# Kernel tuning notes

Measured on AMD Instinct MI355X. Metric: run time of the kernel, lower is better.

The kernel has to match this reference:

```python
import jax, jax.numpy as jnp
import numpy as np

B, T, N, PREV_DIM, CURR_DIM = 8, 32, 500, 200, 128
HEADS, UNITS, MSG_UNITS = 4, 64, 64


def setup_inputs() -> dict:
    key = jax.random.key(0)
    k = jax.random.split(key, 6)
    prev_features = jax.random.normal(k[0], (B, N, PREV_DIM), jnp.float32)
    curr_hidden = jax.random.normal(k[1], (B, T, N, CURR_DIM), jnp.float32)
    # glorot-ish small params
    W_src = jax.random.normal(k[2], (HEADS, PREV_DIM, UNITS), jnp.float32) * 0.05
    W_dst = jax.random.normal(k[3], (HEADS, PREV_DIM, UNITS), jnp.float32) * 0.05
    a = jax.random.normal(k[4], (HEADS, UNITS, 1), jnp.float32) * 0.1
    W_msg = jax.random.normal(k[5], (HEADS, CURR_DIM, MSG_UNITS), jnp.float32) * 0.05
    return {"prev_features": prev_features, "curr_hidden": curr_hidden,
            "W_src": W_src, "W_dst": W_dst, "a": a, "W_msg": W_msg}


def reference(prev_features, curr_hidden, W_src, W_dst, a, W_msg):
    # prev_features: [B, N, Dp]; curr_hidden: [B, T, N, Dc]
    heads = W_src.shape[0]
    head_outputs = []
    for h in range(heads):  # small fixed loop over heads (as in original)
        h_src = jnp.einsum('bnd,du->bnu', prev_features, W_src[h])  # [B,N,U]
        h_dst = jnp.einsum('bnd,du->bnu', prev_features, W_dst[h])  # [B,N,U]
        # GATv2 additive scoring: lrelu(src_i + dst_j) . a   -> [B,N,N]
        pairwise = jax.nn.leaky_relu(h_src[:, :, None, :] + h_dst[:, None, :, :], 0.2)
        scores = jnp.einsum('bnmu,u->bnm', pairwise, a[h, :, 0])
        attn = jax.nn.softmax(scores, axis=-1)  # [B,N,N]; dropout is identity at inference
        msg = jnp.einsum('btnd,du->btnu', curr_hidden, W_msg[h])  # [B,T,N,Mu]
        # same graph applied at every timestep (tf.repeat + batched matmul)
        h_prime = jnp.einsum('bnm,btmu->btnu', attn, msg)  # [B,T,N,Mu]
        head_outputs.append(h_prime)
    return jnp.mean(jnp.stack(head_outputs, axis=-1), axis=-1)
```

## Files before the change

kernel.cpp:

```cpp
#include <hip/hip_runtime.h>

#define B_ 8
#define T_ 32
#define N_ 500
#define DP 200
#define DC 128
#define H_ 4
#define U_ 64
#define NP 512
#define COLS (T_ * U_)
#define K4 (H_ * NP)

typedef __attribute__((ext_vector_type(8))) short bf16x8;
typedef __attribute__((ext_vector_type(4))) float f32x4;

__device__ __forceinline__ ushort f2bf(float f) {
    unsigned u = __float_as_uint(f);
    unsigned r = (u + 0x7FFFu + ((u >> 16) & 1u)) >> 16;
    return (ushort)r;
}

__global__ void zero_fill(uint4* __restrict__ p, int n16) {
    int i = blockIdx.x * blockDim.x + threadIdx.x;
    int stride = gridDim.x * blockDim.x;
    uint4 z; z.x = 0; z.y = 0; z.z = 0; z.w = 0;
    for (; i < n16; i += stride) p[i] = z;
}

__global__ void prep_wT(const float* __restrict__ Wmsg, ushort* __restrict__ WT) {
    int idx = blockIdx.x * 256 + threadIdx.x;
    int h = idx >> 13, u = (idx >> 7) & 63, d = idx & 127;
    WT[idx] = f2bf(0.25f * Wmsg[((size_t)h * DC + d) * U_ + u]);
}

__global__ void __launch_bounds__(512) proj_all(
    const float* __restrict__ prev, const float* __restrict__ Wsrc,
    const float* __restrict__ Wdst, float* __restrict__ hsrc,
    float* __restrict__ hdst)
{
    __shared__ float rows[4 * DP];
    const int tid = threadIdx.x;
    const int bn0 = blockIdx.x * 4;
    for (int e = tid; e < 4 * DP; e += 512) rows[e] = prev[(size_t)bn0 * DP + e];
    __syncthreads();
    const int u = tid & 63;
    const int h = (tid >> 6) & 3;
    const int isdst = tid >> 8;
    const float* W = (isdst ? Wdst : Wsrc) + (size_t)h * DP * U_;
    float a0 = 0.f, a1 = 0.f, a2 = 0.f, a3 = 0.f;
#pragma unroll 4
    for (int d = 0; d < DP; ++d) {
        float w = W[d * U_ + u];
        a0 = fmaf(rows[d], w, a0);
        a1 = fmaf(rows[DP + d], w, a1);
        a2 = fmaf(rows[2 * DP + d], w, a2);
        a3 = fmaf(rows[3 * DP + d], w, a3);
    }
    float acc[4] = {a0, a1, a2, a3};
    float* o = isdst ? hdst : hsrc;
#pragma unroll
    for (int r = 0; r < 4; ++r) {
        int bn = bn0 + r, b = bn / N_, n = bn - b * N_;
        o[(((size_t)b * H_ + h) * N_ + n) * U_ + u] = acc[r];
    }
}

__global__ void __launch_bounds__(512) attn_softmax4(
    const float* __restrict__ hsrc, const float* __restrict__ hdst,
    const float* __restrict__ a_all, ushort* __restrict__ attnB)
{
    const int i0 = blockIdx.x * 4, b = blockIdx.y, h = blockIdx.z;
    const int tid = threadIdx.x;
    __shared__ float s_src[4][U_];
    __shared__ float s_a[U_];
    __shared__ float red[32];
    __shared__ float s_mx[4], s_rs[4];

    if (tid < 256)
        s_src[tid >> 6][tid & 63] =
            hsrc[(((size_t)b * H_ + h) * N_ + i0 + (tid >> 6)) * U_ + (tid & 63)];
    else if (tid < 320)
        s_a[tid - 256] = a_all[h * U_ + (tid - 256)];
    __syncthreads();

    const int j = tid;
    const bool valid = j < N_;
    const float4* dp =
        (const float4*)&hdst[(((size_t)b * H_ + h) * N_ + (valid ? j : 0)) * U_];

    float av0 = 0.f, av1 = 0.f, av2 = 0.f, av3 = 0.f;
    float q = 0.f;
#pragma unroll 1
    for (int kc = 0; kc < 4; ++kc) {
        float4 d0 = dp[kc * 4 + 0];
        float4 d1 = dp[kc * 4 + 1];
        float4 d2 = dp[kc * 4 + 2];
        float4 d3 = dp[kc * 4 + 3];
        float4 a0 = *(const float4*)&s_a[kc * 16 + 0];
        float4 a1 = *(const float4*)&s_a[kc * 16 + 4];
        float4 a2 = *(const float4*)&s_a[kc * 16 + 8];
        float4 a3 = *(const float4*)&s_a[kc * 16 + 12];

        q = fmaf(d0.x, a0.x, q); q = fmaf(d0.y, a0.y, q);
        q = fmaf(d0.z, a0.z, q); q = fmaf(d0.w, a0.w, q);
        q = fmaf(d1.x, a1.x, q); q = fmaf(d1.y, a1.y, q);
        q = fmaf(d1.z, a1.z, q); q = fmaf(d1.w, a1.w, q);
        q = fmaf(d2.x, a2.x, q); q = fmaf(d2.y, a2.y, q);
        q = fmaf(d2.z, a2.z, q); q = fmaf(d2.w, a2.w, q);
        q = fmaf(d3.x, a3.x, q); q = fmaf(d3.y, a3.y, q);
        q = fmaf(d3.z, a3.z, q); q = fmaf(d3.w, a3.w, q);

#pragma unroll
        for (int i = 0; i < 4; ++i) {
            float acc = (i == 0) ? av0 : (i == 1) ? av1 : (i == 2) ? av2 : av3;
            float4 s0 = *(const float4*)&s_src[i][kc * 16 + 0];
            float4 s1 = *(const float4*)&s_src[i][kc * 16 + 4];
            float4 s2 = *(const float4*)&s_src[i][kc * 16 + 8];
            float4 s3 = *(const float4*)&s_src[i][kc * 16 + 12];
            float x;
            x = s0.x + d0.x; acc = fmaf(fabsf(x), a0.x, acc);
            x = s0.y + d0.y; acc = fmaf(fabsf(x), a0.y, acc);
            x = s0.z + d0.z; acc = fmaf(fabsf(x), a0.z, acc);
            x = s0.w + d0.w; acc = fmaf(fabsf(x), a0.w, acc);
            x = s1.x + d1.x; acc = fmaf(fabsf(x), a1.x, acc);
            x = s1.y + d1.y; acc = fmaf(fabsf(x), a1.y, acc);
            x = s1.z + d1.z; acc = fmaf(fabsf(x), a1.z, acc);
            x = s1.w + d1.w; acc = fmaf(fabsf(x), a1.w, acc);
            x = s2.x + d2.x; acc = fmaf(fabsf(x), a2.x, acc);
            x = s2.y + d2.y; acc = fmaf(fabsf(x), a2.y, acc);
            x = s2.z + d2.z; acc = fmaf(fabsf(x), a2.z, acc);
            x = s2.w + d2.w; acc = fmaf(fabsf(x), a2.w, acc);
            x = s3.x + d3.x; acc = fmaf(fabsf(x), a3.x, acc);
            x = s3.y + d3.y; acc = fmaf(fabsf(x), a3.y, acc);
            x = s3.z + d3.z; acc = fmaf(fabsf(x), a3.z, acc);
            x = s3.w + d3.w; acc = fmaf(fabsf(x), a3.w, acc);
            if (i == 0) av0 = acc; else if (i == 1) av1 = acc;
            else if (i == 2) av2 = acc; else av3 = acc;
        }
    }
    const float q6 = 0.6f * q;
    float sc[4];
    sc[0] = valid ? fmaf(0.4f, av0, q6) : -1e30f;
    sc[1] = valid ? fmaf(0.4f, av1, q6) : -1e30f;
    sc[2] = valid ? fmaf(0.4f, av2, q6) : -1e30f;
    sc[3] = valid ? fmaf(0.4f, av3, q6) : -1e30f;

    const int wave = tid >> 6, lane = tid & 63;
#pragma unroll
    for (int i = 0; i < 4; ++i) {
        float m = sc[i];
        for (int off = 1; off < 64; off <<= 1) m = fmaxf(m, __shfl_xor(m, off));
        if (lane == 0) red[wave * 4 + i] = m;
    }
    __syncthreads();
    if (tid < 4) {
        float mm = red[tid];
        for (int w = 1; w < 8; ++w) mm = fmaxf(mm, red[w * 4 + tid]);
        s_mx[tid] = mm;
    }
    __syncthreads();
    float e[4];
#pragma unroll
    for (int i = 0; i < 4; ++i) {
        e[i] = valid ? __expf(sc[i] - s_mx[i]) : 0.f;
        float s = e[i];
        for (int off = 1; off < 64; off <<= 1) s += __shfl_xor(s, off);
        if (lane == 0) red[wave * 4 + i] = s;
    }
    __syncthreads();
    if (tid < 4) {
        float ss = 0.f;
        for (int w = 0; w < 8; ++w) ss += red[w * 4 + tid];
        s_rs[tid] = 1.0f / ss;
    }
    __syncthreads();
    if (valid) {
#pragma unroll
        for (int i = 0; i < 4; ++i)
            attnB[(((size_t)b * H_ + h) * NP + i0 + i) * NP + j] =
                f2bf(e[i] * s_rs[i]);
    }
}

__global__ void __launch_bounds__(256) msg_all(
    const float* __restrict__ curr, const ushort* __restrict__ WT,
    ushort* __restrict__ msgT)
{
    __shared__ ushort As[128 * 136];
    __shared__ ushort Bs[64 * 136];
    const int tid = threadIdx.x;
    const int m0 = blockIdx.x * 128, t = blockIdx.y, b = blockIdx.z;

    const float* cbase = curr + (size_t)(b * T_ + t) * N_ * DC;
#pragma unroll
    for (int it = 0; it < 16; ++it) {
        int e = it * 1024 + tid * 4;
        int r = e >> 7, c = e & 127;
        int gm = m0 + r;
        float4 v; v.x = v.y = v.z = v.w = 0.f;
        if (gm < N_) v = *(const float4*)&cbase[(size_t)gm * DC + c];
        ushort4 o;
        o.x = f2bf(v.x); o.y = f2bf(v.y); o.z = f2bf(v.z); o.w = f2bf(v.w);
        *(ushort4*)&As[r * 136 + c] = o;
    }

    const int wave = tid >> 6, lane = tid & 63;
    const int r15 = lane & 15, quad = lane >> 4;
    const int wm = wave >> 1, wu = wave & 1;

    for (int h = 0; h < H_; ++h) {
        __syncthreads();
#pragma unroll
        for (int it = 0; it < 4; ++it) {
            int e = it * 2048 + tid * 8;
            int u = e >> 7, d = e & 127;
            *(uint4*)&Bs[u * 136 + d] =
                *(const uint4*)&WT[(size_t)h * 8192 + u * 128 + d];
        }
        __syncthreads();

        f32x4 acc[4][2] = {};
#pragma unroll
        for (int ks = 0; ks < 4; ++ks) {
            bf16x8 af[4], bg[2];
#pragma unroll
            for (int f = 0; f < 4; ++f)
                af[f] = *(const bf16x8*)&As[(wm * 64 + f * 16 + r15) * 136 + ks * 32 + quad * 8];
#pragma unroll
            for (int g = 0; g < 2; ++g)
                bg[g] = *(const bf16x8*)&Bs[(wu * 32 + g * 16 + r15) * 136 + ks * 32 + quad * 8];
#pragma unroll
            for (int f = 0; f < 4; ++f)
#pragma unroll
                for (int g = 0; g < 2; ++g)
                    acc[f][g] = __builtin_amdgcn_mfma_f32_16x16x32_bf16(af[f], bg[g], acc[f][g], 0, 0, 0);
        }
#pragma unroll
        for (int f = 0; f < 4; ++f)
#pragma unroll
            for (int g = 0; g < 2; ++g) {
                int m = m0 + wm * 64 + f * 16 + quad * 4;
                int u = wu * 32 + g * 16 + r15;
                int col = t * U_ + u;
                ushort4 o;
                o.x = f2bf(acc[f][g][0]); o.y = f2bf(acc[f][g][1]);
                o.z = f2bf(acc[f][g][2]); o.w = f2bf(acc[f][g][3]);
                *(ushort4*)&msgT[(((size_t)b * H_ + h) * COLS + col) * NP + m] = o;
            }
    }
}

__global__ void __launch_bounds__(256) gemm_big(
    const ushort* __restrict__ msgT, const ushort* __restrict__ attnB,
    float* __restrict__ out)
{
    __shared__ ushort As[128 * 72];
    __shared__ ushort Bs[128 * 72];
    const int tid = threadIdx.x;
    const int mt = blockIdx.x, nt = blockIdx.y, b = blockIdx.z;

    const int wave = tid >> 6, lane = tid & 63;
    const int r15 = lane & 15, quad = lane >> 4;
    const int wm = wave >> 1, wn = wave & 1;
    const int srow = tid >> 3, scol = (tid & 7) * 8;

    f32x4 acc[4][4] = {};
    for (int kk = 0; kk < K4; kk += 64) {
        const int hh = kk >> 9, ko = kk & (NP - 1);
        const ushort* Ab = msgT + (((size_t)b * H_ + hh) * COLS + mt * 128) * NP + ko;
        const ushort* Bb = attnB + (((size_t)b * H_ + hh) * NP + nt * 128) * NP + ko;
#pragma unroll
        for (int r = 0; r < 4; ++r) {
            int row = r * 32 + srow;
            *(uint4*)&As[row * 72 + scol] = *(const uint4*)&Ab[(size_t)row * NP + scol];
            *(uint4*)&Bs[row * 72 + scol] = *(const uint4*)&Bb[(size_t)row * NP + scol];
        }
        __syncthreads();
#pragma unroll
        for (int ks = 0; ks < 2; ++ks) {
            bf16x8 af[4], bg[4];
#pragma unroll
            for (int f = 0; f < 4; ++f)
                af[f] = *(const bf16x8*)&As[(wm * 64 + f * 16 + r15) * 72 + ks * 32 + quad * 8];
#pragma unroll
            for (int g = 0; g < 4; ++g)
                bg[g] = *(const bf16x8*)&Bs[(wn * 64 + g * 16 + r15) * 72 + ks * 32 + quad * 8];
#pragma unroll
            for (int f = 0; f < 4; ++f)
#pragma unroll
                for (int g = 0; g < 4; ++g)
                    acc[f][g] = __builtin_amdgcn_mfma_f32_16x16x32_bf16(af[f], bg[g], acc[f][g], 0, 0, 0);
        }
        __syncthreads();
    }

    const int t = mt * 2 + wm;
#pragma unroll
    for (int f = 0; f < 4; ++f)
#pragma unroll
        for (int g = 0; g < 4; ++g) {
            int u = f * 16 + quad * 4;
            int i = nt * 128 + wn * 64 + g * 16 + r15;
            if (i < N_) {
                float4 v;
                v.x = acc[f][g][0]; v.y = acc[f][g][1];
                v.z = acc[f][g][2]; v.w = acc[f][g][3];
                *(float4*)&out[(((size_t)b * T_ + t) * N_ + i) * U_ + u] = v;
            }
        }
}

__global__ void __launch_bounds__(256) msg_mfma(
    const float* __restrict__ curr, const ushort* __restrict__ WTh,
    ushort* __restrict__ msgT)
{
    __shared__ ushort As[128 * 136];
    __shared__ ushort Bs[64 * 136];
    const int tid = threadIdx.x;
    const int m0 = blockIdx.x * 128, t = blockIdx.y, b = blockIdx.z;

    const float* cbase = curr + (size_t)(b * T_ + t) * N_ * DC;
#pragma unroll
    for (int it = 0; it < 16; ++it) {
        int e = it * 1024 + tid * 4;
        int r = e >> 7, c = e & 127;
        int gm = m0 + r;
        float4 v; v.x = v.y = v.z = v.w = 0.f;
        if (gm < N_) v = *(const float4*)&cbase[(size_t)gm * DC + c];
        ushort4 o;
        o.x = f2bf(v.x); o.y = f2bf(v.y); o.z = f2bf(v.z); o.w = f2bf(v.w);
        *(ushort4*)&As[r * 136 + c] = o;
    }
#pragma unroll
    for (int it = 0; it < 4; ++it) {
        int e = it * 2048 + tid * 8;
        int u = e >> 7, d = e & 127;
        *(uint4*)&Bs[u * 136 + d] = *(const uint4*)&WTh[u * 128 + d];
    }
    __syncthreads();

    const int wave = tid >> 6, lane = tid & 63;
    const int r15 = lane & 15, quad = lane >> 4;
    const int wm = wave >> 1, wu = wave & 1;

    f32x4 acc[4][2] = {};
#pragma unroll
    for (int ks = 0; ks < 4; ++ks) {
        bf16x8 af[4], bg[2];
#pragma unroll
        for (int f = 0; f < 4; ++f)
            af[f] = *(const bf16x8*)&As[(wm * 64 + f * 16 + r15) * 136 + ks * 32 + quad * 8];
#pragma unroll
        for (int g = 0; g < 2; ++g)
            bg[g] = *(const bf16x8*)&Bs[(wu * 32 + g * 16 + r15) * 136 + ks * 32 + quad * 8];
#pragma unroll
        for (int f = 0; f < 4; ++f)
#pragma unroll
            for (int g = 0; g < 2; ++g)
                acc[f][g] = __builtin_amdgcn_mfma_f32_16x16x32_bf16(af[f], bg[g], acc[f][g], 0, 0, 0);
    }
#pragma unroll
    for (int f = 0; f < 4; ++f)
#pragma unroll
        for (int g = 0; g < 2; ++g) {
            int m = m0 + wm * 64 + f * 16 + quad * 4;
            int u = wu * 32 + g * 16 + r15;
            int col = t * U_ + u;
            ushort4 o;
            o.x = f2bf(acc[f][g][0]); o.y = f2bf(acc[f][g][1]);
            o.z = f2bf(acc[f][g][2]); o.w = f2bf(acc[f][g][3]);
            *(ushort4*)&msgT[((size_t)b * COLS + col) * NP + m] = o;
        }
}

__global__ void __launch_bounds__(256) gemm_mfma(
    const ushort* __restrict__ msgT, const ushort* __restrict__ attnB,
    float* __restrict__ out, int h, int init)
{
    __shared__ ushort As[64 * 72];
    __shared__ ushort Bs[64 * 72];
    const int tid = threadIdx.x;
    const int ct = blockIdx.x, it = blockIdx.y, b = blockIdx.z;

    const ushort* Ab = msgT + ((size_t)b * COLS + ct * 64) * NP;
    const ushort* Bb = attnB + (((size_t)b * H_ + h) * NP + it * 64) * NP;

    const int wave = tid >> 6, lane = tid & 63;
    const int r15 = lane & 15, quad = lane >> 4;
    const int wm = wave >> 1, wn = wave & 1;
    const int srow = tid >> 3, scol = (tid & 7) * 8;

    f32x4 acc[2][2] = {};
    for (int kk = 0; kk < NP; kk += 64) {
#pragma unroll
        for (int it2 = 0; it2 < 2; ++it2) {
            int rr = it2 * 32 + srow;
            *(uint4*)&As[rr * 72 + scol] = *(const uint4*)&Ab[(size_t)rr * NP + kk + scol];
            *(uint4*)&Bs[rr * 72 + scol] = *(const uint4*)&Bb[(size_t)rr * NP + kk + scol];
        }
        __syncthreads();
#pragma unroll
        for (int ks = 0; ks < 2; ++ks) {
            bf16x8 af[2], bg[2];
#pragma unroll
            for (int f = 0; f < 2; ++f)
                af[f] = *(const bf16x8*)&As[(wm * 32 + f * 16 + r15) * 72 + ks * 32 + quad * 8];
#pragma unroll
            for (int g = 0; g < 2; ++g)
                bg[g] = *(const bf16x8*)&Bs[(wn * 32 + g * 16 + r15) * 72 + ks * 32 + quad * 8];
#pragma unroll
            for (int f = 0; f < 2; ++f)
#pragma unroll
                for (int g = 0; g < 2; ++g)
                    acc[f][g] = __builtin_amdgcn_mfma_f32_16x16x32_bf16(af[f], bg[g], acc[f][g], 0, 0, 0);
        }
        __syncthreads();
    }

    const int t = ct;
#pragma unroll
    for (int f = 0; f < 2; ++f)
#pragma unroll
        for (int g = 0; g < 2; ++g) {
            int u = wm * 32 + f * 16 + quad * 4;
            int i = it * 64 + wn * 32 + g * 16 + r15;
            if (i < N_) {
                float* op = out + (((size_t)b * T_ + t) * N_ + i) * U_ + u;
                float4 v;
                v.x = acc[f][g][0]; v.y = acc[f][g][1];
                v.z = acc[f][g][2]; v.w = acc[f][g][3];
                if (!init) {
                    float4 old = *(const float4*)op;
                    v.x += old.x; v.y += old.y; v.z += old.z; v.w += old.w;
                }
                *(float4*)op = v;
            }
        }
}

extern "C" void kernel_launch(void* const* d_in, const int* in_sizes, int n_in,
                              void* d_out, int out_size, void* d_ws, size_t ws_size,
                              hipStream_t stream)
{
    const float* prev = (const float*)d_in[0];
    const float* curr = (const float*)d_in[1];
    const float* Wsrc = (const float*)d_in[2];
    const float* Wdst = (const float*)d_in[3];
    const float* avec = (const float*)d_in[4];
    const float* Wmsg = (const float*)d_in[5];
    float* out = (float*)d_out;

    const size_t attnB_b = (size_t)B_ * H_ * NP * NP * 2;
    const size_t msgT4_b = (size_t)B_ * H_ * COLS * NP * 2;
    const size_t msgT1_b = (size_t)B_ * COLS * NP * 2;
    const size_t WT_b    = (size_t)H_ * U_ * DC * 2;
    const size_t hx_b    = (size_t)B_ * H_ * N_ * U_ * 4;

    const bool fused = ws_size >= attnB_b + msgT4_b + WT_b + 2 * hx_b;
    const size_t msg_b = fused ? msgT4_b : msgT1_b;

    ushort* attnB = (ushort*)d_ws;
    ushort* msgT  = (ushort*)((char*)d_ws + attnB_b);
    ushort* WT    = (ushort*)((char*)d_ws + attnB_b + msg_b);
    float*  hsrc  = (float*)((char*)WT + WT_b);
    float*  hdst  = (float*)((char*)hsrc + hx_b);

    zero_fill<<<1024, 256, 0, stream>>>((uint4*)attnB, (int)(attnB_b / 16));
    prep_wT<<<128, 256, 0, stream>>>(Wmsg, WT);
    proj_all<<<1000, 512, 0, stream>>>(prev, Wsrc, Wdst, hsrc, hdst);
    attn_softmax4<<<dim3(125, B_, H_), 512, 0, stream>>>(hsrc, hdst, avec, attnB);

    if (fused) {
        msg_all<<<dim3(4, T_, B_), 256, 0, stream>>>(curr, WT, msgT);
        gemm_big<<<dim3(16, 4, B_), 256, 0, stream>>>(msgT, attnB, out);
    } else {
        for (int h = 0; h < H_; ++h) {
            msg_mfma<<<dim3(4, T_, B_), 256, 0, stream>>>(
                curr, WT + (size_t)h * U_ * DC, msgT);
            gemm_mfma<<<dim3(32, 8, B_), 256, 0, stream>>>(
                msgT, attnB, out, h, h == 0 ? 1 : 0);
        }
    }
}
```

Baseline: 301.6 us.

## Drop attention zero-fill and stage GEMM tiles via direct-to-LDS swizzled loads

The separate zero_fill pass over the padded bf16 attention buffer is removed. The softmax kernel now launches over all 512 padded rows and writes every column itself, zeroing out-of-range source rows. The large GEMM now loads tiles with global_load_lds, which copies global memory straight into shared memory, using an XOR-swizzled unpadded layout in place of the padded register round-trip. This cuts a full-buffer write pass and register staging traffic, but correctness now depends on the unseen score code giving zero weight to padding columns.

```diff
diff --git a/kernel.cpp b/kernel.cpp
--- a/kernel.cpp
+++ b/kernel.cpp
@@ -14,17 +14,17 @@
 typedef __attribute__((ext_vector_type(8))) short bf16x8;
 typedef __attribute__((ext_vector_type(4))) float f32x4;
 
+typedef const __attribute__((address_space(1))) void* gcptr_t;
+typedef __attribute__((address_space(3))) void* lptr_t;
+
+__device__ __forceinline__ void async16(const void* g, void* lds) {
+    __builtin_amdgcn_global_load_lds((gcptr_t)g, (lptr_t)lds, 16, 0, 0);
+}
+
 __device__ __forceinline__ ushort f2bf(float f) {
     unsigned u = __float_as_uint(f);
     unsigned r = (u + 0x7FFFu + ((u >> 16) & 1u)) >> 16;
     return (ushort)r;
-}
-
-__global__ void zero_fill(uint4* __restrict__ p, int n16) {
-    int i = blockIdx.x * blockDim.x + threadIdx.x;
-    int stride = gridDim.x * blockDim.x;
-    uint4 z; z.x = 0; z.y = 0; z.z = 0; z.w = 0;
-    for (; i < n16; i += stride) p[i] = z;
 }
 
 __global__ void prep_wT(const float* __restrict__ Wmsg, ushort* __restrict__ WT) {
@@ -65,7 +65,7 @@
     }
 }
 
-__global__ void __launch_bounds__(512) attn_softmax4(
+__global__ void __launch_bounds__(512) attn_softmax6(
     const float* __restrict__ hsrc, const float* __restrict__ hdst,
     const float* __restrict__ a_all, ushort* __restrict__ attnB)
 {
@@ -76,10 +76,11 @@
     __shared__ float red[32];
     __shared__ float s_mx[4], s_rs[4];
 
-    if (tid < 256)
-        s_src[tid >> 6][tid & 63] =
-            hsrc[(((size_t)b * H_ + h) * N_ + i0 + (tid >> 6)) * U_ + (tid & 63)];
-    else if (tid < 320)
+    if (tid < 256) {
+        int gi = i0 + (tid >> 6);
+        s_src[tid >> 6][tid & 63] = (gi < N_) ?
+            hsrc[(((size_t)b * H_ + h) * N_ + gi) * U_ + (tid & 63)] : 0.f;
+    } else if (tid < 320)
         s_a[tid - 256] = a_all[h * U_ + (tid - 256)];
     __syncthreads();
 
@@ -162,7 +163,7 @@
     float e[4];
 #pragma unroll
     for (int i = 0; i < 4; ++i) {
-        e[i] = valid ? __expf(sc[i] - s_mx[i]) : 0.f;
+        e[i] = __expf(sc[i] - s_mx[i]);
         float s = e[i];
         for (int off = 1; off < 64; off <<= 1) s += __shfl_xor(s, off);
         if (lane == 0) red[wave * 4 + i] = s;
@@ -174,12 +175,10 @@
         s_rs[tid] = 1.0f / ss;
     }
     __syncthreads();
-    if (valid) {
-#pragma unroll
-        for (int i = 0; i < 4; ++i)
-            attnB[(((size_t)b * H_ + h) * NP + i0 + i) * NP + j] =
-                f2bf(e[i] * s_rs[i]);
-    }
+#pragma unroll
+    for (int i = 0; i < 4; ++i)
+        attnB[(((size_t)b * H_ + h) * NP + i0 + i) * NP + j] =
+            f2bf(e[i] * s_rs[i]);
 }
 
 __global__ void __launch_bounds__(256) msg_all(
@@ -250,19 +249,19 @@
     }
 }
 
-__global__ void __launch_bounds__(256) gemm_big(
+__global__ void __launch_bounds__(256) gemm_big2(
     const ushort* __restrict__ msgT, const ushort* __restrict__ attnB,
     float* __restrict__ out)
 {
-    __shared__ ushort As[128 * 72];
-    __shared__ ushort Bs[128 * 72];
+    __shared__ ushort As[128 * 64];
+    __shared__ ushort Bs[128 * 64];
     const int tid = threadIdx.x;
     const int mt = blockIdx.x, nt = blockIdx.y, b = blockIdx.z;
 
     const int wave = tid >> 6, lane = tid & 63;
     const int r15 = lane & 15, quad = lane >> 4;
     const int wm = wave >> 1, wn = wave & 1;
-    const int srow = tid >> 3, scol = (tid & 7) * 8;
+    const int lrow = lane >> 3, lch = lane & 7;
 
     f32x4 acc[4][4] = {};
     for (int kk = 0; kk < K4; kk += 64) {
@@ -270,21 +269,29 @@
         const ushort* Ab = msgT + (((size_t)b * H_ + hh) * COLS + mt * 128) * NP + ko;
         const ushort* Bb = attnB + (((size_t)b * H_ + hh) * NP + nt * 128) * NP + ko;
 #pragma unroll
-        for (int r = 0; r < 4; ++r) {
-            int row = r * 32 + srow;
-            *(uint4*)&As[row * 72 + scol] = *(const uint4*)&Ab[(size_t)row * NP + scol];
-            *(uint4*)&Bs[row * 72 + scol] = *(const uint4*)&Bb[(size_t)row * NP + scol];
+        for (int l = 0; l < 4; ++l) {
+            const int R0 = wave * 32 + l * 8;
+            const int row = R0 + lrow;
+            const int gch = lch ^ (row & 7);
+            async16(Ab + (size_t)row * NP + gch * 8, &As[R0 * 64]);
+            async16(Bb + (size_t)row * NP + gch * 8, &Bs[R0 * 64]);
         }
         __syncthreads();
 #pragma unroll
         for (int ks = 0; ks < 2; ++ks) {
             bf16x8 af[4], bg[4];
 #pragma unroll
-            for (int f = 0; f < 4; ++f)
-                af[f] = *(const bf16x8*)&As[(wm * 64 + f * 16 + r15) * 72 + ks * 32 + quad * 8];
-#pragma unroll
-            for (int g = 0; g < 4; ++g)
-                bg[g] = *(const bf16x8*)&Bs[(wn * 64 + g * 16 + r15) * 72 + ks * 32 + quad * 8];
+            for (int f = 0; f < 4; ++f) {
+                int row = wm * 64 + f * 16 + r15;
+                int c = (ks * 4 + quad) ^ (row & 7);
+                af[f] = *(const bf16x8*)&As[row * 64 + c * 8];
+            }
+#pragma unroll
+            for (int g = 0; g < 4; ++g) {
+                int row = wn * 64 + g * 16 + r15;
+                int c = (ks * 4 + quad) ^ (row & 7);
+                bg[g] = *(const bf16x8*)&Bs[row * 64 + c * 8];
+            }
 #pragma unroll
             for (int f = 0; f < 4; ++f)
 #pragma unroll
@@ -465,14 +472,13 @@
     float*  hsrc  = (float*)((char*)WT + WT_b);
     float*  hdst  = (float*)((char*)hsrc + hx_b);
 
-    zero_fill<<<1024, 256, 0, stream>>>((uint4*)attnB, (int)(attnB_b / 16));
     prep_wT<<<128, 256, 0, stream>>>(Wmsg, WT);
     proj_all<<<1000, 512, 0, stream>>>(prev, Wsrc, Wdst, hsrc, hdst);
-    attn_softmax4<<<dim3(125, B_, H_), 512, 0, stream>>>(hsrc, hdst, avec, attnB);
+    attn_softmax6<<<dim3(128, B_, H_), 512, 0, stream>>>(hsrc, hdst, avec, attnB);
 
     if (fused) {
         msg_all<<<dim3(4, T_, B_), 256, 0, stream>>>(curr, WT, msgT);
-        gemm_big<<<dim3(16, 4, B_), 256, 0, stream>>>(msgT, attnB, out);
+        gemm_big2<<<dim3(16, 4, B_), 256, 0, stream>>>(msgT, attnB, out);
     } else {
         for (int h = 0; h < H_; ++h) {
             msg_mfma<<<dim3(4, T_, B_), 256, 0, stream>>>(
```

Result: no change. 297.7 us (-1.3%).
